# Kernel optimization log

Measured on AMD Instinct MI355X. Metric: run time of the kernel, lower is better.

The kernel has to match this reference:

```python
import jax, jax.numpy as jnp
import numpy as np

B, N, DIM = 2, 2048, 512
H, DH = 8, 64
INNER = H * DH
SCALE = DH ** -0.5


def setup_inputs() -> dict:
    key = jax.random.key(0)
    ks = jax.random.split(key, 8)
    s = 0.02
    return {
        "nodes": jax.random.normal(ks[0], (B, N, DIM), dtype=jnp.float32),
        "edge_mask": jax.random.bernoulli(ks[1], 0.9, (B, N, N)),
        "wq": jax.random.normal(ks[2], (DIM, INNER), dtype=jnp.float32) * s,
        "bq": jnp.zeros((INNER,), dtype=jnp.float32),
        "wkv": jax.random.normal(ks[3], (DIM, 2 * INNER), dtype=jnp.float32) * s,
        "bkv": jnp.zeros((2 * INNER,), dtype=jnp.float32),
        "wo": jax.random.normal(ks[4], (INNER, DIM), dtype=jnp.float32) * s,
        "bo": jnp.zeros((DIM,), dtype=jnp.float32),
    }


def reference(nodes, edge_mask, wq, bq, wkv, bkv, wo, bo):
    b, n, _ = nodes.shape
    q = nodes @ wq + bq                      # [b, n, h*dh]
    kv = nodes @ wkv + bkv                   # [b, n, 2*h*dh]
    k, v = jnp.split(kv, 2, axis=-1)
    # split heads -> [b, h, n, dh]
    split = lambda t: t.reshape(b, n, H, DH).transpose(0, 2, 1, 3)
    q, k, v = split(q), split(k), split(v)
    sim = jnp.einsum('bhid,bhjd->bhij', q, k) * SCALE
    max_neg = -jnp.finfo(sim.dtype).max
    sim = jnp.where(edge_mask[:, None, :, :], sim, max_neg)
    attn = jax.nn.softmax(sim, axis=-1)
    out = jnp.einsum('bhij,bhjd->bhid', attn, v)      # [b, h, n, dh]
    out = out.transpose(0, 2, 1, 3).reshape(b, n, INNER)
    return out @ wo + bo
```

## Files before the change

### kernel.cpp

```cpp
#include <hip/hip_runtime.h>
#include <cstdint>
#include <cstddef>

#define DEVI __device__ __forceinline__

typedef __bf16 bf16x8 __attribute__((ext_vector_type(8)));
typedef float floatx4 __attribute__((ext_vector_type(4)));
typedef unsigned short us4v __attribute__((ext_vector_type(4)));
typedef unsigned short us8 __attribute__((ext_vector_type(8)));

static_assert(sizeof(bf16x8) == 16, "bf16x8 must be 16B");
static_assert(sizeof(us8) == 16, "us8 must be 16B");


#if __has_builtin(__builtin_amdgcn_cvt_pk_bf16_f32)
DEVI unsigned short f2bf(float f) {
  typedef __bf16 bf16x2 __attribute__((ext_vector_type(2)));
  union { bf16x2 v; unsigned short u[2]; } c;
  c.v = __builtin_amdgcn_cvt_pk_bf16_f32(f, 0.f);
  return c.u[0];
}
#else
DEVI unsigned short f2bf(float f) {
  unsigned int u = __float_as_uint(f);
  u += 0x7fffu + ((u >> 16) & 1u);
  return (unsigned short)(u >> 16);
}
#endif

DEVI float exp2c(float x) {
#if __has_builtin(__builtin_amdgcn_exp2f)
  return __builtin_amdgcn_exp2f(x);
#else
  return exp2f(x);
#endif
}

DEVI bf16x8 ld8(const unsigned short* p) { return *(const bf16x8*)p; }

typedef const __attribute__((address_space(1))) void* gas_ptr;
typedef __attribute__((address_space(3))) void* las_ptr;

DEVI void gld16(const void* g, void* l) {
  __builtin_amdgcn_global_load_lds((gas_ptr)g, (las_ptr)l, 16, 0, 0);
}

#define WAIT_LGKM0() __builtin_amdgcn_s_waitcnt(0xc07f)

__global__ __launch_bounds__(256) void prep_k(
    const float* __restrict__ nodes, const void* __restrict__ mask,
    const float* __restrict__ wq, const float* __restrict__ wkv,
    const float* __restrict__ wo,
    unsigned short* __restrict__ XB, unsigned short* __restrict__ WQKVT,
    unsigned short* __restrict__ WOT, unsigned int* __restrict__ pm) {
  int bid = blockIdx.x;
  if (bid < 8192) {
    __shared__ int mode;
    const unsigned int* md = (const unsigned int*)mask;
    unsigned int probe = md[threadIdx.x];
    bool odd = (probe > 1u && probe != 0x3f800000u);
    if (threadIdx.x == 0) mode = 0;
    __syncthreads();
    if (odd) atomicOr(&mode, 1);
    __syncthreads();
    int byteMode = mode;
    int t = bid * 256 + threadIdx.x;
    int lane = threadIdx.x & 63;
    unsigned int n;
    if (byteMode) {
      unsigned int x = md[t];
      n = ((x & 0xffu) ? 1u : 0u) | ((x & 0xff00u) ? 2u : 0u) |
          ((x & 0xff0000u) ? 4u : 0u) | ((x >> 24) ? 8u : 0u);
    } else {
      uint4 v = ((const uint4*)mask)[t];
      n = (v.x ? 1u : 0u) | (v.y ? 2u : 0u) | (v.z ? 4u : 0u) | (v.w ? 8u : 0u);
    }
    unsigned int w = n << ((lane & 7) * 4);
    w |= __shfl_xor(w, 1);
    w |= __shfl_xor(w, 2);
    w |= __shfl_xor(w, 4);
    if ((lane & 7) == 0) pm[t >> 3] = w;
  } else if (bid < 10240) {
    int i = (bid - 8192) * 256 + threadIdx.x;
    float4 v = ((const float4*)nodes)[i];
    us4v o;
    o[0] = f2bf(v.x); o[1] = f2bf(v.y); o[2] = f2bf(v.z); o[3] = f2bf(v.w);
    *(us4v*)(XB + (size_t)i * 4) = o;
  } else {
    int tb = bid - 10240;
    int x = tb & 15, y = (tb >> 4) & 7, z = tb >> 7;
    const float* src; unsigned short* dst; int C, c0;
    if (z == 0)      { if (x >= 8) return; src = wq;  dst = WQKVT; C = 512;  c0 = 0; }
    else if (z == 1) { src = wkv; dst = WQKVT; C = 1024; c0 = 512; }
    else             { if (x >= 8) return; src = wo;  dst = WOT;  C = 512;  c0 = 0; }
    __shared__ unsigned short t2[64 * 64];
    const int t = threadIdx.x;
    const int ct = x * 64, rt = y * 64;
    for (int p = 0; p < 4; p++) {
      int kl = p * 16 + (t >> 4);
      int cc = (t & 15) * 4;
      float4 v = *(const float4*)&src[(size_t)(rt + kl) * C + ct + cc];
      float f[4] = {v.x, v.y, v.z, v.w};
      for (int i = 0; i < 4; i++) {
        int c = cc + i;
        t2[c * 64 + (kl ^ (c & 56))] = f2bf(f[i]);
      }
    }
    __syncthreads();
    for (int p = 0; p < 2; p++) {
      int c = p * 32 + (t >> 3);
      int kc = (t & 7) * 8;
      us8 v = *(const us8*)&t2[c * 64 + (kc ^ (c & 56))];
      *(us8*)&dst[(size_t)(c0 + ct + c) * 512 + rt + kc] = v;
    }
  }
}

__global__ __launch_bounds__(256) void gemm_qkv_k(
    const unsigned short* __restrict__ A,
    const unsigned short* __restrict__ Bt,
    const float* __restrict__ bq, const float* __restrict__ bkv,
    unsigned short* __restrict__ Qo, unsigned short* __restrict__ Ko,
    unsigned short* __restrict__ VTo) {
  __shared__ unsigned short smem[8192];
  unsigned short* sA = smem;
  unsigned short* sB = smem + 2048;
  const int tid = threadIdx.x;
  const int wave = tid >> 6, lane = tid & 63, quad = lane >> 4, l16 = lane & 15;
  const int wm = wave >> 1, wn = wave & 1;
  const int bm = blockIdx.x, bn = blockIdx.y;
  floatx4 acc[2][4] = {};
  const int arow = lane >> 2;
  const int ag = lane & 3;
  for (int kt = 0; kt < 16; kt++) {
    __syncthreads();
    {
      int rowA = wave * 16 + arow;
      int gA = ag ^ (rowA & 3);
      gld16(&A[(size_t)(bm * 64 + rowA) * 512 + kt * 32 + gA * 8], &sA[(wave * 16) * 32]);
      for (int p = 0; p < 2; p++) {
        int rowB = p * 64 + wave * 16 + arow;
        int gB = ag ^ (rowB & 3);
        gld16(&Bt[(size_t)(bn * 128 + rowB) * 512 + kt * 32 + gB * 8],
              &sB[(p * 64 + wave * 16) * 32]);
      }
    }
    __syncthreads();
    bf16x8 aF[2], bF[4];
    int swz = (quad ^ (l16 & 3)) * 8;
    for (int i = 0; i < 2; i++) aF[i] = ld8(&sA[(wm * 32 + i * 16 + l16) * 32 + swz]);
    for (int j = 0; j < 4; j++) bF[j] = ld8(&sB[(wn * 64 + j * 16 + l16) * 32 + swz]);
    for (int i = 0; i < 2; i++)
      for (int j = 0; j < 4; j++)
        acc[i][j] = __builtin_amdgcn_mfma_f32_16x16x32_bf16(aF[i], bF[j], acc[i][j], 0, 0, 0);
  }

  const int sec = bn * 2 + wn;
  float bias[4];
  float scale = 1.0f;
  if (sec < 8) {
    for (int j = 0; j < 4; j++) bias[j] = bq[sec * 64 + j * 16 + l16];
    scale = 0.18033688011112042f;
  } else {
    for (int j = 0; j < 4; j++) bias[j] = bkv[(sec - 8) * 64 + j * 16 + l16];
  }
  const int gr0 = bm * 64 + wm * 32;
  const int b = gr0 >> 11, n0 = gr0 & 2047;
  unsigned short* pw = smem + wave * 2048;
  __syncthreads();
  if (sec < 16) {
    for (int i = 0; i < 2; i++)
      for (int j = 0; j < 4; j++) {
        int cg = j * 2 + (l16 >> 3), ci = l16 & 7;
        for (int r = 0; r < 4; r++) {
          int row = i * 16 + quad * 4 + r;
          pw[row * 64 + ((cg ^ (row & 7)) * 8) + ci] = f2bf((acc[i][j][r] + bias[j]) * scale);
        }
      }
    WAIT_LGKM0();
    unsigned short* dst = (sec < 8) ? Qo + ((size_t)(b * 8 + sec) * 2048 + n0) * 64
                                    : Ko + ((size_t)(b * 8 + sec - 8) * 2048 + n0) * 64;
    for (int p = 0; p < 4; p++) {
      int row = p * 8 + (lane >> 3);
      int c8 = lane & 7;
      us8 v = *(const us8*)&pw[row * 64 + ((c8 ^ (row & 7)) * 8)];
      *(us8*)&dst[(size_t)row * 64 + c8 * 8] = v;
    }
  } else {
    for (int i = 0; i < 2; i++)
      for (int j = 0; j < 4; j++) {
        int d = j * 16 + l16;
        us4v t;
        for (int r = 0; r < 4; r++) t[r] = f2bf(acc[i][j][r] + bias[j]);
        *(us4v*)&pw[d * 32 + ((quad ^ (d & 3)) * 8) + i * 4] = t;
      }
    WAIT_LGKM0();
    unsigned short* dst = VTo + (size_t)(b * 8 + sec - 16) * 64 * 2048 + n0;
    for (int p = 0; p < 4; p++) {
      int d = p * 16 + (lane >> 2);
      int c4 = lane & 3;
      us8 v = *(const us8*)&pw[d * 32 + ((c4 ^ (d & 3)) * 8)];
      *(us8*)&dst[(size_t)d * 2048 + c4 * 8] = v;
    }
  }
}

__global__ __launch_bounds__(256, 2) void attn_k(
    const unsigned short* __restrict__ Q,
    const unsigned short* __restrict__ K,
    const unsigned short* __restrict__ Vt,
    const unsigned int* __restrict__ pm,
    unsigned short* __restrict__ AO) {
  __shared__ unsigned short kT[4][4096];
  __shared__ unsigned short vT[4][4096];
  __shared__ float lsumB[4][64];
  const int tid = threadIdx.x;
  const int wave = tid >> 6, lane = tid & 63, quad = lane >> 4, l16 = lane & 15;
  const int bh = blockIdx.x, qt = blockIdx.y, b = bh >> 3, h = bh & 7;
  const int q0 = qt * 64;
  const unsigned short* Qb = Q + (size_t)bh * 2048 * 64;
  const unsigned short* Kb = K + (size_t)bh * 2048 * 64;
  const unsigned short* Vb = Vt + (size_t)bh * 64 * 2048;
  const unsigned int* pmB = pm + (size_t)b * 2048 * 64;

  bf16x8 qF[4][2];
  for (int qb = 0; qb < 4; qb++) {
    qF[qb][0] = ld8(&Qb[(size_t)(q0 + qb * 16 + l16) * 64 + quad * 8]);
    qF[qb][1] = ld8(&Qb[(size_t)(q0 + qb * 16 + l16) * 64 + 32 + quad * 8]);
  }

  floatx4 oacc[4][4] = {};
  float lsum[4] = {0.f, 0.f, 0.f, 0.f};

  const int srow = lane >> 3;
  const int gK = (lane & 7) ^ srow;
  const int rsw0 = quad ^ (l16 & 7);
  const int rsw1 = (4 + quad) ^ (l16 & 7);

  for (int it = 0; it < 8; ++it) {
    const int k0w = it * 256 + wave * 64;
    for (int p = 0; p < 8; p++) {
      gld16(&Kb[(size_t)(k0w + p * 8 + srow) * 64 + gK * 8], &kT[wave][p * 512]);
      gld16(&Vb[(size_t)(p * 8 + srow) * 2048 + k0w + gK * 8], &vT[wave][p * 512]);
    }
    uint2 mw[4];
    for (int qb = 0; qb < 4; qb++)
      mw[qb] = *(const uint2*)&pmB[(size_t)(q0 + qb * 16 + l16) * 64 + it * 8 + wave * 2];
    __syncthreads();

    for (int c = 0; c < 2; c++) {
      floatx4 st[4][2];
      for (int k2 = 0; k2 < 2; k2++) {
        const unsigned short* kr = &kT[wave][((c * 2 + k2) * 16 + l16) * 64];
        bf16x8 kf0 = ld8(kr + rsw0 * 8);
        bf16x8 kf1 = ld8(kr + rsw1 * 8);
        for (int qb = 0; qb < 4; qb++) {
          floatx4 z = {0.f, 0.f, 0.f, 0.f};
          z = __builtin_amdgcn_mfma_f32_16x16x32_bf16(kf0, qF[qb][0], z, 0, 0, 0);
          st[qb][k2] = __builtin_amdgcn_mfma_f32_16x16x32_bf16(kf1, qF[qb][1], z, 0, 0, 0);
        }
      }
      union uB { bf16x8 v; unsigned short u[8]; } pf[4];
      for (int qb = 0; qb < 4; qb++) {
        unsigned int w = c ? mw[qb].y : mw[qb].x;
        for (int k2 = 0; k2 < 2; k2++) {
          int base = k2 * 16 + quad * 4;
          for (int r = 0; r < 4; r++) {
            float e = exp2c(st[qb][k2][r]);
            e = ((w >> (base + r)) & 1u) ? e : 0.f;
            lsum[qb] += e;
            pf[qb].u[k2 * 4 + r] = f2bf(e);
          }
        }
      }
      for (int db = 0; db < 4; db++) {
        int row = db * 16 + l16;
        bf16x8 va = ld8(&vT[wave][row * 64 + (((c * 4 + quad) ^ (row & 7)) * 8)]);
        for (int qb = 0; qb < 4; qb++)
          oacc[db][qb] =
              __builtin_amdgcn_mfma_f32_16x16x32_bf16(va, pf[qb].v, oacc[db][qb], 0, 0, 0);
      }
    }
    __syncthreads();
  }

  for (int qb = 0; qb < 4; qb++) {
    lsum[qb] += __shfl_xor(lsum[qb], 16);
    lsum[qb] += __shfl_xor(lsum[qb], 32);
  }
  lsumB[wave][quad * 16 + l16] = lsum[quad];

  float* pO = (float*)&kT[0][0];
  float* myR = pO + wave * 4096;
  for (int db = 0; db < 4; db++)
    for (int qb = 0; qb < 4; qb++) {
      int q = qb * 16 + l16;
      *(floatx4*)&myR[q * 64 + (((db * 4 + quad) ^ l16) & 15) * 4] = oacc[db][qb];
    }
  __syncthreads();
  {
    int q = tid >> 2, dblk = tid & 3;
    float inv = 1.0f / (lsumB[0][q] + lsumB[1][q] + lsumB[2][q] + lsumB[3][q]);
    float o[16];
    for (int i = 0; i < 4; i++) {
      int dg = dblk * 4 + i;
      int off = q * 64 + ((dg ^ q) & 15) * 4;
      floatx4 s = *(floatx4*)&pO[off];
      s += *(floatx4*)&pO[4096 + off];
      s += *(floatx4*)&pO[8192 + off];
      s += *(floatx4*)&pO[12288 + off];
      for (int r = 0; r < 4; r++) o[i * 4 + r] = s[r] * inv;
    }
    us8 v0, v1;
    for (int i = 0; i < 8; i++) { v0[i] = f2bf(o[i]); v1[i] = f2bf(o[8 + i]); }
    unsigned short* dst = &AO[((size_t)b * 2048 + q0 + q) * 512 + h * 64 + dblk * 16];
    *(us8*)dst = v0;
    *(us8*)(dst + 8) = v1;
  }
}

__global__ __launch_bounds__(256) void gemm_out_k(
    const unsigned short* __restrict__ A,
    const unsigned short* __restrict__ Bt,
    const float* __restrict__ bo, float* __restrict__ out) {
  __shared__ unsigned short smem[6144];
  unsigned short* sA = smem;
  unsigned short* sB = smem + 2048;
  const int tid = threadIdx.x;
  const int wave = tid >> 6, lane = tid & 63, quad = lane >> 4, l16 = lane & 15;
  const int wm = wave >> 1, wn = wave & 1;
  const int bm = blockIdx.x, bn = blockIdx.y;
  floatx4 acc[2][4] = {};
  const int arow = lane >> 2;
  const int ag = lane & 3;
  for (int kt = 0; kt < 16; kt++) {
    __syncthreads();
    {
      int rowA = wave * 16 + arow;
      int gA = ag ^ (rowA & 3);
      gld16(&A[(size_t)(bm * 64 + rowA) * 512 + kt * 32 + gA * 8], &sA[(wave * 16) * 32]);
      for (int p = 0; p < 2; p++) {
        int rowB = p * 64 + wave * 16 + arow;
        int gB = ag ^ (rowB & 3);
        gld16(&Bt[(size_t)(bn * 128 + rowB) * 512 + kt * 32 + gB * 8],
              &sB[(p * 64 + wave * 16) * 32]);
      }
    }
    __syncthreads();
    bf16x8 aF[2], bF[4];
    int swz = (quad ^ (l16 & 3)) * 8;
    for (int i = 0; i < 2; i++) aF[i] = ld8(&sA[(wm * 32 + i * 16 + l16) * 32 + swz]);
    for (int j = 0; j < 4; j++) bF[j] = ld8(&sB[(wn * 64 + j * 16 + l16) * 32 + swz]);
    for (int i = 0; i < 2; i++)
      for (int j = 0; j < 4; j++)
        acc[i][j] = __builtin_amdgcn_mfma_f32_16x16x32_bf16(aF[i], bF[j], acc[i][j], 0, 0, 0);
  }
  for (int i = 0; i < 2; i++)
    for (int j = 0; j < 4; j++) {
      int gc = bn * 128 + wn * 64 + j * 16 + l16;
      float bb = bo[gc];
      for (int r = 0; r < 4; r++) {
        int gr = bm * 64 + wm * 32 + i * 16 + quad * 4 + r;
        out[(size_t)gr * 512 + gc] = acc[i][j][r] + bb;
      }
    }
}

extern "C" void kernel_launch(void* const* d_in, const int* in_sizes, int n_in,
                              void* d_out, int out_size, void* d_ws, size_t ws_size,
                              hipStream_t stream) {
  const float* nodes = (const float*)d_in[0];
  const void*  mask  = d_in[1];
  const float* wq    = (const float*)d_in[2];
  const float* bq    = (const float*)d_in[3];
  const float* wkv   = (const float*)d_in[4];
  const float* bkv   = (const float*)d_in[5];
  const float* wo    = (const float*)d_in[6];
  const float* bo    = (const float*)d_in[7];
  float* out = (float*)d_out;

  char* ws = (char*)d_ws;
  unsigned short* XB    = (unsigned short*)(ws + 0);
  unsigned short* WQKVT = (unsigned short*)(ws + 4194304);
  unsigned short* WOT   = (unsigned short*)(ws + 5767168);
  unsigned short* Qm    = (unsigned short*)(ws + 6291456);
  unsigned short* Km    = (unsigned short*)(ws + 10485760);
  unsigned short* VTm   = (unsigned short*)(ws + 18874368);
  unsigned short* AOm   = (unsigned short*)(ws + 23068672);
  unsigned int*   PM    = (unsigned int*)(ws + 27262976);

  prep_k<<<10624, 256, 0, stream>>>(nodes, mask, wq, wkv, wo, XB, WQKVT, WOT, PM);
  gemm_qkv_k<<<dim3(64, 12), 256, 0, stream>>>(XB, WQKVT, bq, bkv, Qm, Km, VTm);
  attn_k<<<dim3(16, 32), 256, 0, stream>>>(Qm, Km, VTm, PM, AOm);
  gemm_out_k<<<dim3(64, 4), 256, 0, stream>>>(AOm, WOT, bo, out);
}
```

Before: 155.2 us.

## Double-buffer per-wave K/V tiles and compute row sums via MFMA

The attention loop now gives each wave its own K/V tile and double-buffers it. The next 32-key chunk is prefetched with global_load_lds while the current one is processed, and manual vmcnt waits replace the block-wide __syncthreads. The softmax denominator is now accumulated by an MFMA against a vector of ones instead of scalar adds and shuffles, and MFMA sections run at raised wave priority. This aims to hide load latency and cut VALU work. It relies on hand-coded waitcnt values being correct for the issued load count.

Result: no change. 152.5 us (-1.7%).

```diff
diff --git a/kernel.cpp b/kernel.cpp
--- a/kernel.cpp
+++ b/kernel.cpp
@@ -46,6 +46,9 @@
 }
 
 #define WAIT_LGKM0() __builtin_amdgcn_s_waitcnt(0xc07f)
+#define WAIT_VM12()  __builtin_amdgcn_s_waitcnt(0x0f7c)
+#define WAIT_VM0()   __builtin_amdgcn_s_waitcnt(0x0f70)
+#define SB()         __builtin_amdgcn_sched_barrier(0)
 
 __global__ __launch_bounds__(256) void prep_k(
     const float* __restrict__ nodes, const void* __restrict__ mask,
@@ -211,8 +214,7 @@
     const unsigned short* __restrict__ Vt,
     const unsigned int* __restrict__ pm,
     unsigned short* __restrict__ AO) {
-  __shared__ unsigned short kT[4][4096];
-  __shared__ unsigned short vT[4][4096];
+  __shared__ unsigned short kv[2][4][4096];
   __shared__ float lsumB[4][64];
   const int tid = threadIdx.x;
   const int wave = tid >> 6, lane = tid & 63, quad = lane >> 4, l16 = lane & 15;
@@ -224,75 +226,126 @@
   const unsigned int* pmB = pm + (size_t)b * 2048 * 64;
 
   bf16x8 qF[4][2];
+#pragma unroll
   for (int qb = 0; qb < 4; qb++) {
     qF[qb][0] = ld8(&Qb[(size_t)(q0 + qb * 16 + l16) * 64 + quad * 8]);
     qF[qb][1] = ld8(&Qb[(size_t)(q0 + qb * 16 + l16) * 64 + 32 + quad * 8]);
   }
 
   floatx4 oacc[4][4] = {};
-  float lsum[4] = {0.f, 0.f, 0.f, 0.f};
+  floatx4 lsacc[4] = {};
+
+  union { us8 u; bf16x8 v; } onesU;
+#pragma unroll
+  for (int i = 0; i < 8; i++) onesU.u[i] = 0x3f80;
+  const bf16x8 onesF = onesU.v;
 
   const int srow = lane >> 3;
   const int gK = (lane & 7) ^ srow;
+  const int dV = lane >> 2;
+  const int gV = (lane & 3) ^ (dV & 3);
   const int rsw0 = quad ^ (l16 & 7);
   const int rsw1 = (4 + quad) ^ (l16 & 7);
 
-  for (int it = 0; it < 8; ++it) {
-    const int k0w = it * 256 + wave * 64;
-    for (int p = 0; p < 8; p++) {
-      gld16(&Kb[(size_t)(k0w + p * 8 + srow) * 64 + gK * 8], &kT[wave][p * 512]);
-      gld16(&Vb[(size_t)(p * 8 + srow) * 2048 + k0w + gK * 8], &vT[wave][p * 512]);
-    }
-    uint2 mw[4];
+  unsigned short* kv0 = &kv[0][wave][0];
+  unsigned short* kv1 = &kv[1][wave][0];
+
+  struct MW { unsigned int w[4]; };
+  MW mwA, mwB;
+
+  auto prefetch = [&](int it, unsigned short* dst, MW& mw) {
+    const int k0w = it * 128 + wave * 32;
+#pragma unroll
     for (int qb = 0; qb < 4; qb++)
-      mw[qb] = *(const uint2*)&pmB[(size_t)(q0 + qb * 16 + l16) * 64 + it * 8 + wave * 2];
-    __syncthreads();
-
-    for (int c = 0; c < 2; c++) {
-      floatx4 st[4][2];
+      mw.w[qb] = pmB[(size_t)(q0 + qb * 16 + l16) * 64 + it * 4 + wave];
+#pragma unroll
+    for (int p = 0; p < 4; p++) {
+      gld16(&Kb[(size_t)(k0w + p * 8 + srow) * 64 + gK * 8], dst + p * 512);
+      gld16(&Vb[(size_t)(p * 16 + dV) * 2048 + k0w + gV * 8], dst + 2048 + p * 512);
+    }
+  };
+
+  auto step = [&](const unsigned short* buf, const MW& mw) {
+    floatx4 st[4][2];
+    __builtin_amdgcn_s_setprio(1);
+#pragma unroll
+    for (int k2 = 0; k2 < 2; k2++) {
+      const unsigned short* kr = &buf[(k2 * 16 + l16) * 64];
+      bf16x8 kf0 = ld8(kr + rsw0 * 8);
+      bf16x8 kf1 = ld8(kr + rsw1 * 8);
+#pragma unroll
+      for (int qb = 0; qb < 4; qb++) {
+        floatx4 z = {0.f, 0.f, 0.f, 0.f};
+        z = __builtin_amdgcn_mfma_f32_16x16x32_bf16(kf0, qF[qb][0], z, 0, 0, 0);
+        st[qb][k2] = __builtin_amdgcn_mfma_f32_16x16x32_bf16(kf1, qF[qb][1], z, 0, 0, 0);
+      }
+    }
+    __builtin_amdgcn_s_setprio(0);
+    union uB { bf16x8 v; unsigned short u[8]; } pf[4];
+#pragma unroll
+    for (int qb = 0; qb < 4; qb++) {
+      unsigned int w = mw.w[qb];
+#pragma unroll
       for (int k2 = 0; k2 < 2; k2++) {
-        const unsigned short* kr = &kT[wave][((c * 2 + k2) * 16 + l16) * 64];
-        bf16x8 kf0 = ld8(kr + rsw0 * 8);
-        bf16x8 kf1 = ld8(kr + rsw1 * 8);
-        for (int qb = 0; qb < 4; qb++) {
-          floatx4 z = {0.f, 0.f, 0.f, 0.f};
-          z = __builtin_amdgcn_mfma_f32_16x16x32_bf16(kf0, qF[qb][0], z, 0, 0, 0);
-          st[qb][k2] = __builtin_amdgcn_mfma_f32_16x16x32_bf16(kf1, qF[qb][1], z, 0, 0, 0);
+#pragma unroll
+        for (int r = 0; r < 4; r++) {
+          float e = exp2c(st[qb][k2][r]);
+          e = ((w >> (k2 * 16 + quad * 4 + r)) & 1u) ? e : 0.f;
+          pf[qb].u[k2 * 4 + r] = f2bf(e);
         }
       }
-      union uB { bf16x8 v; unsigned short u[8]; } pf[4];
-      for (int qb = 0; qb < 4; qb++) {
-        unsigned int w = c ? mw[qb].y : mw[qb].x;
-        for (int k2 = 0; k2 < 2; k2++) {
-          int base = k2 * 16 + quad * 4;
-          for (int r = 0; r < 4; r++) {
-            float e = exp2c(st[qb][k2][r]);
-            e = ((w >> (base + r)) & 1u) ? e : 0.f;
-            lsum[qb] += e;
-            pf[qb].u[k2 * 4 + r] = f2bf(e);
-          }
-        }
-      }
-      for (int db = 0; db < 4; db++) {
-        int row = db * 16 + l16;
-        bf16x8 va = ld8(&vT[wave][row * 64 + (((c * 4 + quad) ^ (row & 7)) * 8)]);
-        for (int qb = 0; qb < 4; qb++)
-          oacc[db][qb] =
-              __builtin_amdgcn_mfma_f32_16x16x32_bf16(va, pf[qb].v, oacc[db][qb], 0, 0, 0);
-      }
-    }
-    __syncthreads();
-  }
-
-  for (int qb = 0; qb < 4; qb++) {
-    lsum[qb] += __shfl_xor(lsum[qb], 16);
-    lsum[qb] += __shfl_xor(lsum[qb], 32);
-  }
-  lsumB[wave][quad * 16 + l16] = lsum[quad];
-
-  float* pO = (float*)&kT[0][0];
+    }
+    __builtin_amdgcn_s_setprio(1);
+#pragma unroll
+    for (int qb = 0; qb < 4; qb++)
+      lsacc[qb] = __builtin_amdgcn_mfma_f32_16x16x32_bf16(onesF, pf[qb].v, lsacc[qb], 0, 0, 0);
+#pragma unroll
+    for (int db = 0; db < 4; db++) {
+      const int d = db * 16 + l16;
+      bf16x8 va = ld8(&buf[2048 + d * 32 + ((quad ^ (d & 3)) * 8)]);
+#pragma unroll
+      for (int qb = 0; qb < 4; qb++)
+        oacc[db][qb] =
+            __builtin_amdgcn_mfma_f32_16x16x32_bf16(va, pf[qb].v, oacc[db][qb], 0, 0, 0);
+    }
+    __builtin_amdgcn_s_setprio(0);
+  };
+
+  SB();
+  prefetch(0, kv0, mwA);
+  SB();
+#pragma unroll 1
+  for (int i = 0; i < 8; ++i) {
+    prefetch(i * 2 + 1, kv1, mwB);
+    SB();
+    WAIT_VM12();
+    SB();
+    step(kv0, mwA);
+    SB();
+    if (i < 7) {
+      prefetch(i * 2 + 2, kv0, mwA);
+      SB();
+      WAIT_VM12();
+      SB();
+    } else {
+      WAIT_VM0();
+      SB();
+    }
+    step(kv1, mwB);
+    SB();
+  }
+
+  if (quad == 0) {
+#pragma unroll
+    for (int qb = 0; qb < 4; qb++) lsumB[wave][qb * 16 + l16] = lsacc[qb][0];
+  }
+  __syncthreads();
+
+  float* pO = (float*)&kv[0][0][0];
   float* myR = pO + wave * 4096;
+#pragma unroll
   for (int db = 0; db < 4; db++)
+#pragma unroll
     for (int qb = 0; qb < 4; qb++) {
       int q = qb * 16 + l16;
       *(floatx4*)&myR[q * 64 + (((db * 4 + quad) ^ l16) & 15) * 4] = oacc[db][qb];
```
